# Performance work log

Hardware: AMD Instinct MI355X
Metric: run time of the kernel (lower is better)

## Reference

```python
import jax, jax.numpy as jnp
import numpy as np

TEMPERATURE = 0.5
N, D = 8192, 256
N_CLASSES = 64


def setup_inputs() -> dict:
    key = jax.random.key(0)
    k1, k2 = jax.random.split(key)
    emb = jax.random.normal(k1, (N, D), dtype=jnp.float32)
    # original module expects normalized embeddings
    emb = emb / jnp.linalg.norm(emb, axis=-1, keepdims=True)
    labels = jax.random.randint(k2, (N,), 0, N_CLASSES, dtype=jnp.int64)
    return {"embeddings": emb, "epitope_labels": labels}


def reference(embeddings, epitope_labels):
    n = embeddings.shape[0]
    # [N, N] pairwise similarities
    sim = jnp.matmul(embeddings, embeddings.T) / TEMPERATURE
    eye = jnp.eye(n, dtype=bool)
    labels_eq = epitope_labels[None, :] == epitope_labels[:, None]
    mask_pos = labels_eq & ~eye  # positives exclude self
    # row-max subtraction (detached, matches torch .detach())
    sim_max = jax.lax.stop_gradient(jnp.max(sim, axis=1, keepdims=True))
    shifted = sim - sim_max
    exp_sim = jnp.exp(shifted)
    # denominator excludes the diagonal (self-similarity)
    denom = jnp.sum(jnp.where(eye, 0.0, exp_sim), axis=1)  # [N]
    # per-pair loss: -log(exp_sim_ij / denom_i) = -(shifted_ij - log denom_i)
    per_pair = -(shifted - jnp.log(denom)[:, None])
    # mean over positive pairs (equivalent to masked_select + repeat_interleave + mean)
    n_pos = jnp.sum(mask_pos)
    loss = jnp.sum(jnp.where(mask_pos, per_pair, 0.0)) / n_pos
    return loss
```

## Files before the change

### kernel.cpp

```cpp
#include <hip/hip_runtime.h>
#include <hip/hip_bf16.h>

#define N 8192
#define D 256
#define NC 64
#define NQ 16
#define NT 16

typedef __attribute__((ext_vector_type(8))) short bf16x8;
typedef __attribute__((ext_vector_type(4))) float f32x4;

#define K1 2.8853900817779268f
#define K2 (-2.8853900817779268f)

__device__ inline unsigned short f2bf(float x) {
    __hip_bfloat16 h = __float2bfloat16(x);
    return *reinterpret_cast<unsigned short*>(&h);
}

__device__ inline float fast_exp2(float t) {
#if __has_builtin(__builtin_amdgcn_exp2f)
    return __builtin_amdgcn_exp2f(t);
#else
    return __expf(t * 0.69314718056f);
#endif
}

__global__ void convert_kernel(const float4* __restrict__ E4, ushort4* __restrict__ Ebf4) {
    int i = blockIdx.x * blockDim.x + threadIdx.x;
    if (i < (N * D) / 4) {
        float4 v = E4[i];
        ushort4 o;
        o.x = f2bf(v.x); o.y = f2bf(v.y); o.z = f2bf(v.z); o.w = f2bf(v.w);
        Ebf4[i] = o;
    }
}

__global__ __launch_bounds__(256, 2)
void sim_kernel(const __hip_bfloat16* __restrict__ Ebf,
                const int* __restrict__ labels,
                float* __restrict__ Zp, float* __restrict__ Pp) {
    __shared__ unsigned char Bsh[3 * 16384];
    __shared__ int Lcol[512];

    const int tid  = threadIdx.x;
    const int lane = tid & 63;
    const int wid  = tid >> 6;
    const int l15  = lane & 15;
    const int l4   = lane >> 4;
    const int rpnl = blockIdx.x >> 4;
    const int q    = blockIdx.x & 15;
    const char* eb = (const char*)Ebf;

    {
        int i0 = tid * 2;
        Lcol[i0]     = labels[q * 512 + i0];
        Lcol[i0 + 1] = labels[q * 512 + i0 + 1];
    }

    bf16x8 a[4][8];
#pragma unroll
    for (int rg = 0; rg < 4; ++rg) {
        int row = rpnl * 256 + wid * 64 + rg * 16 + l15;
        const char* ap = eb + (size_t)row * 512 + l4 * 16;
#pragma unroll
        for (int kg = 0; kg < 8; ++kg)
            a[rg][kg] = *reinterpret_cast<const bf16x8*>(ap + kg * 64);
    }

    int labP[4];
#pragma unroll
    for (int rg = 0; rg < 4; ++rg) {
        int rr = rpnl * 256 + wid * 64 + rg * 16 + l4 * 4;
        labP[rg] = labels[rr] | (labels[rr + 1] << 8) |
                   (labels[rr + 2] << 16) | (labels[rr + 3] << 24);
    }

    __syncthreads();

    const unsigned laneSwz = (unsigned)(l15 * 64 + ((l4 ^ ((l15 >> 1) & 3)) << 4));

    auto stage = [&](int t, int buf) {
        const unsigned bufb = (unsigned)buf * 16384u;
#pragma unroll
        for (int m = 0; m < 4; ++m) {
            int c = wid * 4 + m;
            int kg = c >> 1, colblk = c & 1;
            int colLocal = colblk * 16 + (lane >> 2);
            int seg = (lane & 3) ^ ((colLocal >> 1) & 3);
            const char* src = eb + (size_t)(q * 512 + t * 32 + colLocal) * 512
                            + kg * 64 + seg * 16;
            __builtin_amdgcn_global_load_lds(
                (const __attribute__((address_space(1))) void*)src,
                (__attribute__((address_space(3))) void*)
                    (Bsh + bufb + kg * 2048u + colblk * 1024u),
                16, 0, 0);
        }
    };

    float zacc[4][4], pacc[4][4];
#pragma unroll
    for (int rg = 0; rg < 4; ++rg)
#pragma unroll
        for (int r = 0; r < 4; ++r) { zacc[rg][r] = 0.0f; pacc[rg][r] = 0.0f; }

    stage(0, 0);
    stage(1, 1);

    int bcur = 0;
    for (int t = 0; t < NT; ++t) {
        if (t < NT - 1) { asm volatile("s_waitcnt vmcnt(4)" ::: "memory"); }
        else            { asm volatile("s_waitcnt vmcnt(0)" ::: "memory"); }
        __builtin_amdgcn_s_barrier();
        if (t + 2 < NT) {
            int bs = bcur + 2; if (bs >= 3) bs -= 3;
            stage(t + 2, bs);
        }

        const unsigned bufb = (unsigned)bcur * 16384u;
        f32x4 acc[4][2];
#pragma unroll
        for (int rg = 0; rg < 4; ++rg) {
            acc[rg][0] = (f32x4){0.f, 0.f, 0.f, 0.f};
            acc[rg][1] = (f32x4){0.f, 0.f, 0.f, 0.f};
        }

        __builtin_amdgcn_s_setprio(1);
#pragma unroll
        for (int kg = 0; kg < 8; ++kg) {
            bf16x8 b0 = *reinterpret_cast<const bf16x8*>(Bsh + bufb + kg * 2048 + laneSwz);
            bf16x8 b1 = *reinterpret_cast<const bf16x8*>(Bsh + bufb + kg * 2048 + 1024 + laneSwz);
#pragma unroll
            for (int rg = 0; rg < 4; ++rg) {
                acc[rg][0] = __builtin_amdgcn_mfma_f32_16x16x32_bf16(a[rg][kg], b0, acc[rg][0], 0, 0, 0);
                acc[rg][1] = __builtin_amdgcn_mfma_f32_16x16x32_bf16(a[rg][kg], b1, acc[rg][1], 0, 0, 0);
            }
        }
        __builtin_amdgcn_s_setprio(0);

        int labj0 = Lcol[t * 32 + l15];
        int labj1 = Lcol[t * 32 + 16 + l15];
#pragma unroll
        for (int rg = 0; rg < 4; ++rg)
#pragma unroll
            for (int r = 0; r < 4; ++r) {
                int li = (labP[rg] >> (r * 8)) & 255;
                float d0 = acc[rg][0][r], d1 = acc[rg][1][r];
                zacc[rg][r] += fast_exp2(__builtin_fmaf(d0, K1, K2))
                             + fast_exp2(__builtin_fmaf(d1, K1, K2));
                pacc[rg][r] += ((li == labj0) ? d0 : 0.0f)
                             + ((li == labj1) ? d1 : 0.0f);
            }

        bcur += 1; if (bcur >= 3) bcur -= 3;
    }

#pragma unroll
    for (int rg = 0; rg < 4; ++rg)
#pragma unroll
        for (int r = 0; r < 4; ++r) {
            float z = zacc[rg][r], pw = pacc[rg][r];
#pragma unroll
            for (int m = 1; m <= 8; m <<= 1) {
                z  += __shfl_xor(z, m, 64);
                pw += __shfl_xor(pw, m, 64);
            }
            if (l15 == 0) {
                int row = rpnl * 256 + wid * 64 + rg * 16 + l4 * 4 + r;
                Zp[q * N + row] = z;
                Pp[q * N + row] = pw;
            }
        }
}

__global__ __launch_bounds__(1024)
void finalize_kernel(const float* __restrict__ Zp, const float* __restrict__ Pp,
                     const int* __restrict__ labels, float* __restrict__ out) {
    __shared__ int hist[NC];
    __shared__ float s0[1024], s1[1024];
    const int t = threadIdx.x;
    if (t < NC) hist[t] = 0;
    __syncthreads();
    for (int i = t; i < N; i += 1024) atomicAdd(&hist[labels[i]], 1);
    __syncthreads();

    float num = 0.0f, den = 0.0f;
    for (int i = t; i < N; i += 1024) {
        float z = 0.0f, pv = 0.0f;
#pragma unroll
        for (int qq = 0; qq < NQ; ++qq) {
            z  += Zp[qq * N + i];
            pv += Pp[qq * N + i];
        }
        z -= 1.0f;
        pv = 2.0f * (pv - 1.0f);
        float c = (float)(hist[labels[i]] - 1);
        num += c * (2.0f + __logf(z)) - pv;
        den += c;
    }
    s0[t] = num; s1[t] = den;
    __syncthreads();
    for (int s = 512; s > 0; s >>= 1) {
        if (t < s) { s0[t] += s0[t + s]; s1[t] += s1[t + s]; }
        __syncthreads();
    }
    if (t == 0) out[0] = s0[0] / s1[0];
}

extern "C" void kernel_launch(void* const* d_in, const int* in_sizes, int n_in,
                              void* d_out, int out_size, void* d_ws, size_t ws_size,
                              hipStream_t stream) {
    const float* emb  = (const float*)d_in[0];
    const int* labels = (const int*)d_in[1];
    float* out = (float*)d_out;

    char* ws = (char*)d_ws;
    __hip_bfloat16* Ebf = (__hip_bfloat16*)ws;
    float* Zp = (float*)(ws + (size_t)N * D * 2);
    float* Pp = Zp + NQ * N;

    convert_kernel<<<(N * D / 4 + 255) / 256, 256, 0, stream>>>(
        (const float4*)emb, (ushort4*)Ebf);
    sim_kernel<<<512, 256, 0, stream>>>(Ebf, labels, Zp, Pp);
    finalize_kernel<<<1, 1024, 0, stream>>>(Zp, Pp, labels, out);
}
```

Baseline: 114.2 us.

## Compute positive-pair sum via per-class embedding sums instead of in-GEMM masking

Replaces the label-masked accumulation of positive similarities inside the GEMM epilogue with an algebraic identity: the sum of same-class dot products equals the sum of squared norms of per-class embedding sums. A new class-sum kernel builds partial per-class sums and a global histogram, and finalize is parallelized across 32 blocks with atomic accumulation plus a tiny divide kernel. The sim kernel drops its label loads, LDS label table and select work, and moves from a 3-deep to a 4-deep LDS pipeline. This adds two extra launches and a serial class-sum pass, and uses bf16-rounded embeddings for the positive term.

Result: slower. 156.0 us (+36.6%).

```diff
diff --git a/kernel.cpp b/kernel.cpp
--- a/kernel.cpp
+++ b/kernel.cpp
@@ -26,7 +26,13 @@
 #endif
 }
 
-__global__ void convert_kernel(const float4* __restrict__ E4, ushort4* __restrict__ Ebf4) {
+__device__ inline float bf2f(unsigned short u) {
+    unsigned v = ((unsigned)u) << 16;
+    return __builtin_bit_cast(float, v);
+}
+
+__global__ void convert_kernel(const float4* __restrict__ E4, ushort4* __restrict__ Ebf4,
+                               float* __restrict__ nd, int* __restrict__ histg) {
     int i = blockIdx.x * blockDim.x + threadIdx.x;
     if (i < (N * D) / 4) {
         float4 v = E4[i];
@@ -34,14 +40,46 @@
         o.x = f2bf(v.x); o.y = f2bf(v.y); o.z = f2bf(v.z); o.w = f2bf(v.w);
         Ebf4[i] = o;
     }
+    if (i < 2) nd[i] = 0.0f;
+    if (i < NC) histg[i] = 0;
+}
+
+__global__ __launch_bounds__(256)
+void classsum_kernel(const __hip_bfloat16* __restrict__ Ebf,
+                     const int* __restrict__ labels,
+                     float* __restrict__ Spart, int* __restrict__ histg) {
+    const int t = threadIdx.x;
+    const int c = t >> 2;
+    const int dseg = t & 3;
+    const int b = blockIdx.x;
+    float acc[64];
+#pragma unroll
+    for (int k = 0; k < 64; ++k) acc[k] = 0.0f;
+    int cnt = 0;
+    for (int r = 0; r < 128; ++r) {
+        int i = b * 128 + r;
+        if (labels[i] == c) {
+            ++cnt;
+            const bf16x8* rp = reinterpret_cast<const bf16x8*>(
+                (const unsigned short*)Ebf + (size_t)i * D + dseg * 64);
+#pragma unroll
+            for (int v8 = 0; v8 < 8; ++v8) {
+                bf16x8 v = rp[v8];
+#pragma unroll
+                for (int e = 0; e < 8; ++e)
+                    acc[v8 * 8 + e] += bf2f((unsigned short)v[e]);
+            }
+        }
+    }
+    float* dst = Spart + (size_t)b * (NC * D) + c * D + dseg * 64;
+#pragma unroll
+    for (int k = 0; k < 64; ++k) dst[k] = acc[k];
+    if (dseg == 0 && cnt) atomicAdd(&histg[c], cnt);
 }
 
 __global__ __launch_bounds__(256, 2)
-void sim_kernel(const __hip_bfloat16* __restrict__ Ebf,
-                const int* __restrict__ labels,
-                float* __restrict__ Zp, float* __restrict__ Pp) {
-    __shared__ unsigned char Bsh[3 * 16384];
-    __shared__ int Lcol[512];
+void sim_kernel(const __hip_bfloat16* __restrict__ Ebf, float* __restrict__ Zp) {
+    __shared__ unsigned char Bsh[4 * 16384];
 
     const int tid  = threadIdx.x;
     const int lane = tid & 63;
@@ -52,12 +90,6 @@
     const int q    = blockIdx.x & 15;
     const char* eb = (const char*)Ebf;
 
-    {
-        int i0 = tid * 2;
-        Lcol[i0]     = labels[q * 512 + i0];
-        Lcol[i0 + 1] = labels[q * 512 + i0 + 1];
-    }
-
     bf16x8 a[4][8];
 #pragma unroll
     for (int rg = 0; rg < 4; ++rg) {
@@ -67,16 +99,11 @@
         for (int kg = 0; kg < 8; ++kg)
             a[rg][kg] = *reinterpret_cast<const bf16x8*>(ap + kg * 64);
     }
-
-    int labP[4];
-#pragma unroll
-    for (int rg = 0; rg < 4; ++rg) {
-        int rr = rpnl * 256 + wid * 64 + rg * 16 + l4 * 4;
-        labP[rg] = labels[rr] | (labels[rr + 1] << 8) |
-                   (labels[rr + 2] << 16) | (labels[rr + 3] << 24);
-    }
-
-    __syncthreads();
+#pragma unroll
+    for (int rg = 0; rg < 4; ++rg)
+#pragma unroll
+        for (int kg = 0; kg < 8; ++kg)
+            asm volatile("" : "+v"(a[rg][kg]));
 
     const unsigned laneSwz = (unsigned)(l15 * 64 + ((l4 ^ ((l15 >> 1) & 3)) << 4));
 
@@ -98,26 +125,22 @@
         }
     };
 
-    float zacc[4][4], pacc[4][4];
+    float zacc[4][4];
 #pragma unroll
     for (int rg = 0; rg < 4; ++rg)
 #pragma unroll
-        for (int r = 0; r < 4; ++r) { zacc[rg][r] = 0.0f; pacc[rg][r] = 0.0f; }
+        for (int r = 0; r < 4; ++r) zacc[rg][r] = 0.0f;
 
     stage(0, 0);
     stage(1, 1);
-
-    int bcur = 0;
+    stage(2, 2);
+
     for (int t = 0; t < NT; ++t) {
-        if (t < NT - 1) { asm volatile("s_waitcnt vmcnt(4)" ::: "memory"); }
-        else            { asm volatile("s_waitcnt vmcnt(0)" ::: "memory"); }
+        asm volatile("s_waitcnt vmcnt(8)" ::: "memory");
         __builtin_amdgcn_s_barrier();
-        if (t + 2 < NT) {
-            int bs = bcur + 2; if (bs >= 3) bs -= 3;
-            stage(t + 2, bs);
-        }
-
-        const unsigned bufb = (unsigned)bcur * 16384u;
+        if (t + 3 < NT) stage(t + 3, (t + 3) & 3);
+
+        const unsigned bufb = (unsigned)(t & 3) * 16384u;
         f32x4 acc[4][2];
 #pragma unroll
         for (int rg = 0; rg < 4; ++rg) {
@@ -138,73 +161,65 @@
         }
         __builtin_amdgcn_s_setprio(0);
 
-        int labj0 = Lcol[t * 32 + l15];
-        int labj1 = Lcol[t * 32 + 16 + l15];
 #pragma unroll
         for (int rg = 0; rg < 4; ++rg)
 #pragma unroll
-            for (int r = 0; r < 4; ++r) {
-                int li = (labP[rg] >> (r * 8)) & 255;
-                float d0 = acc[rg][0][r], d1 = acc[rg][1][r];
-                zacc[rg][r] += fast_exp2(__builtin_fmaf(d0, K1, K2))
-                             + fast_exp2(__builtin_fmaf(d1, K1, K2));
-                pacc[rg][r] += ((li == labj0) ? d0 : 0.0f)
-                             + ((li == labj1) ? d1 : 0.0f);
-            }
-
-        bcur += 1; if (bcur >= 3) bcur -= 3;
+            for (int r = 0; r < 4; ++r)
+                zacc[rg][r] += fast_exp2(__builtin_fmaf(acc[rg][0][r], K1, K2))
+                             + fast_exp2(__builtin_fmaf(acc[rg][1][r], K1, K2));
     }
 
 #pragma unroll
     for (int rg = 0; rg < 4; ++rg)
 #pragma unroll
         for (int r = 0; r < 4; ++r) {
-            float z = zacc[rg][r], pw = pacc[rg][r];
-#pragma unroll
-            for (int m = 1; m <= 8; m <<= 1) {
-                z  += __shfl_xor(z, m, 64);
-                pw += __shfl_xor(pw, m, 64);
-            }
+            float z = zacc[rg][r];
+#pragma unroll
+            for (int m = 1; m <= 8; m <<= 1) z += __shfl_xor(z, m, 64);
             if (l15 == 0) {
                 int row = rpnl * 256 + wid * 64 + rg * 16 + l4 * 4 + r;
                 Zp[q * N + row] = z;
-                Pp[q * N + row] = pw;
             }
         }
 }
 
-__global__ __launch_bounds__(1024)
-void finalize_kernel(const float* __restrict__ Zp, const float* __restrict__ Pp,
-                     const int* __restrict__ labels, float* __restrict__ out) {
-    __shared__ int hist[NC];
-    __shared__ float s0[1024], s1[1024];
+__global__ __launch_bounds__(256)
+void finalize_kernel(const float* __restrict__ Zp, const float* __restrict__ Spart,
+                     const int* __restrict__ labels, const int* __restrict__ histg,
+                     float* __restrict__ nd) {
+    __shared__ float s0[256], s1[256];
     const int t = threadIdx.x;
-    if (t < NC) hist[t] = 0;
-    __syncthreads();
-    for (int i = t; i < N; i += 1024) atomicAdd(&hist[labels[i]], 1);
-    __syncthreads();
-
-    float num = 0.0f, den = 0.0f;
-    for (int i = t; i < N; i += 1024) {
-        float z = 0.0f, pv = 0.0f;
-#pragma unroll
-        for (int qq = 0; qq < NQ; ++qq) {
-            z  += Zp[qq * N + i];
-            pv += Pp[qq * N + i];
-        }
-        z -= 1.0f;
-        pv = 2.0f * (pv - 1.0f);
-        float c = (float)(hist[labels[i]] - 1);
-        num += c * (2.0f + __logf(z)) - pv;
-        den += c;
-    }
+    const int b = blockIdx.x;
+
+    int i = b * 256 + t;
+    float z = 0.0f;
+#pragma unroll
+    for (int qq = 0; qq < NQ; ++qq) z += Zp[qq * N + i];
+    z -= 1.0f;
+    float c = (float)(histg[labels[i]] - 1);
+    float num = c * (2.0f + __logf(z));
+    float den = c;
+
+#pragma unroll
+    for (int u = 0; u < 2; ++u) {
+        int pidx = b * 512 + t * 2 + u;
+        float s = 0.0f;
+        for (int bb = 0; bb < 64; ++bb) s += Spart[(size_t)bb * (NC * D) + pidx];
+        num -= 2.0f * s * s;
+    }
+    if (b == 0 && t == 0) num += 2.0f * (float)N;
+
     s0[t] = num; s1[t] = den;
     __syncthreads();
-    for (int s = 512; s > 0; s >>= 1) {
+    for (int s = 128; s > 0; s >>= 1) {
         if (t < s) { s0[t] += s0[t + s]; s1[t] += s1[t + s]; }
         __syncthreads();
     }
-    if (t == 0) out[0] = s0[0] / s1[0];
+    if (t == 0) { atomicAdd(&nd[0], s0[0]); atomicAdd(&nd[1], s1[0]); }
+}
+
+__global__ void div_kernel(const float* __restrict__ nd, float* __restrict__ out) {
+    out[0] = nd[0] / nd[1];
 }
 
 extern "C" void kernel_launch(void* const* d_in, const int* in_sizes, int n_in,
@@ -216,11 +231,15 @@
 
     char* ws = (char*)d_ws;
     __hip_bfloat16* Ebf = (__hip_bfloat16*)ws;
-    float* Zp = (float*)(ws + (size_t)N * D * 2);
-    float* Pp = Zp + NQ * N;
+    float* Zp    = (float*)(ws + (size_t)N * D * 2);
+    float* Spart = Zp + NQ * N;
+    float* nd    = Spart + 64 * (NC * D);
+    int*   histg = (int*)(nd + 2);
 
     convert_kernel<<<(N * D / 4 + 255) / 256, 256, 0, stream>>>(
-        (const float4*)emb, (ushort4*)Ebf);
-    sim_kernel<<<512, 256, 0, stream>>>(Ebf, labels, Zp, Pp);
-    finalize_kernel<<<1, 1024, 0, stream>>>(Zp, Pp, labels, out);
-}
+        (const float4*)emb, (ushort4*)Ebf, nd, histg);
+    classsum_kernel<<<64, 256, 0, stream>>>(Ebf, labels, Spart, histg);
+    sim_kernel<<<512, 256, 0, stream>>>(Ebf, Zp);
+    finalize_kernel<<<32, 256, 0, stream>>>(Zp, Spart, labels, histg, nd);
+    div_kernel<<<1, 1, 0, stream>>>(nd, out);
+}
```
